# Optimization experiments

Measured on AMD Instinct MI355X. Metric: run time of the kernel, lower is better.

The kernel has to match this reference:

```python
import jax, jax.numpy as jnp
import numpy as np

B, N, IN_F, OUT_F, H = 4, 2048, 256, 256, 8
NH = OUT_F // H  # 32
SLOPE = 0.2
NEG_INF = -9e15


def setup_inputs() -> dict:
    key = jax.random.key(0)
    k1, k2, k3, k4 = jax.random.split(key, 4)
    h = jax.random.normal(k1, (B, N, IN_F), jnp.float32)
    adj = jax.random.randint(k2, (B, N, N), 0, 2).astype(jnp.int32)
    # xavier_uniform with gain 1.414
    gw = 1.414 * np.sqrt(6.0 / (IN_F + H * NH))
    W = jax.random.uniform(k3, (IN_F, H * NH), jnp.float32, -gw, gw)
    ga = 1.414 * np.sqrt(6.0 / (2 * NH + 1))
    a = jax.random.uniform(k4, (2 * NH, 1), jnp.float32, -ga, ga)
    return {"h": h, "adj": adj, "W": W, "a": a}


def reference(h, adj, W, a):
    Wh = h @ W                              # [B, N, H*NH]
    # Faithful to torch .view: raw memory reinterpretation, not a transpose.
    Wh = Wh.reshape(B, H, N, NH)            # [B, H, N, NH]
    Wh1 = Wh @ a[:NH]                       # [B, H, N, 1]
    Wh2 = Wh @ a[NH:]                       # [B, H, N, 1]
    e = Wh1 + jnp.swapaxes(Wh2, 2, 3)       # [B, H, N, N] additive scores
    e = jnp.where(e >= 0, e, SLOPE * e)     # leaky relu
    e = jnp.where(adj[:, None] > 0, e, NEG_INF)
    attn = jax.nn.softmax(e, axis=-1)       # [B, H, N, N]
    h_prime = attn @ Wh                     # [B, H, N, NH]
    h_prime = h_prime.reshape(B, N, OUT_F)  # raw reshape, matches torch .view
    return jax.nn.elu(h_prime)
```

## Files before the change

### kernel.cpp

```cpp
#include <hip/hip_runtime.h>
#include <hip/hip_bf16.h>

#define B_    4
#define N_    2048
#define INF_  256
#define OUTF_ 256
#define H_    8
#define NH_   32
#define BH_   (B_ * H_)
#define ROWS_ (B_ * N_)
#define VSZ_  (N_ * NH_)

typedef float  f32x4 __attribute__((ext_vector_type(4)));
typedef short  s16x8 __attribute__((ext_vector_type(8)));

static __device__ __forceinline__ short f2bf(float x) {
    union { __hip_bfloat16 b; unsigned short u; } cv;
    cv.b = __float2bfloat16(x);
    return (short)cv.u;
}

__global__ __launch_bounds__(256) void hwconv(const float* __restrict__ h,
                                              const float* __restrict__ W,
                                              short* __restrict__ hb,
                                              short* __restrict__ Wf) {
    const int t = blockIdx.x * 256 + threadIdx.x;
    if (blockIdx.x < 1024) {
        const float4* src = (const float4*)(h + (size_t)t * 8);
        float4 v0 = src[0], v1 = src[1];
        float vv[8] = {v0.x, v0.y, v0.z, v0.w, v1.x, v1.y, v1.z, v1.w};
        s16x8 o;
#pragma unroll
        for (int i = 0; i < 8; ++i) o[i] = f2bf(vv[i]);
        *(s16x8*)(hb + (size_t)t * 8) = o;
    } else {
        const int u = t - 1024 * 256;
        const int lane = u & 63, nf = (u >> 6) & 15, kt = u >> 10;
        const float* src = W + (size_t)(kt * 32 + (lane >> 4) * 8) * 256 +
                           nf * 16 + (lane & 15);
        s16x8 o;
#pragma unroll
        for (int i = 0; i < 8; ++i) o[i] = f2bf(src[(size_t)i * 256]);
        *(s16x8*)(Wf + (size_t)u * 8) = o;
    }
}

__global__ __launch_bounds__(256) void gemm_mfma(const short* __restrict__ hb,
                                                 const short* __restrict__ Wf,
                                                 float* __restrict__ Wh) {
    const int bm  = blockIdx.x * 64;
    const int bn4 = blockIdx.y * 4;
    const int tid = threadIdx.x;
    const int wv = tid >> 6, l = tid & 63;
    const int lr = l & 15, lg = l >> 4;
    const int arow = bm + wv * 16 + lr;

    f32x4 acc[4] = {};
    const s16x8* wf = (const s16x8*)Wf;
    const s16x8* ha = (const s16x8*)(hb + (size_t)arow * 256 + lg * 8);

#pragma unroll
    for (int kt = 0; kt < 8; ++kt) {
        s16x8 a = ha[kt * 4];
#pragma unroll
        for (int nf = 0; nf < 4; ++nf) {
            s16x8 b = wf[(size_t)(kt * 16 + bn4 + nf) * 64 + l];
            acc[nf] = __builtin_amdgcn_mfma_f32_16x16x32_bf16(a, b, acc[nf], 0, 0, 0);
        }
    }
#pragma unroll
    for (int nf = 0; nf < 4; ++nf)
#pragma unroll
        for (int r = 0; r < 4; ++r)
            Wh[(size_t)(bm + wv * 16 + 4 * lg + r) * 256 +
               (size_t)(bn4 + nf) * 16 + lr] = acc[nf][r];
}

__global__ __launch_bounds__(256) void st_kernel(const float* __restrict__ Wh,
                                                 const float* __restrict__ a,
                                                 float* __restrict__ s,
                                                 float* __restrict__ t) {
    const int row = blockIdx.x * 256 + threadIdx.x;
    const float* v = Wh + (size_t)row * NH_;
    float s_ = 0.f, t_ = 0.f;
#pragma unroll
    for (int k = 0; k < NH_; k += 4) {
        float4 vv = *(const float4*)(v + k);
        float4 a1 = *(const float4*)(a + k);
        float4 a2 = *(const float4*)(a + NH_ + k);
        s_ += vv.x * a1.x + vv.y * a1.y + vv.z * a1.z + vv.w * a1.w;
        t_ += vv.x * a2.x + vv.y * a2.y + vv.z * a2.z + vv.w * a2.w;
    }
    s[row] = s_;
    t[row] = t_;
}

__global__ __launch_bounds__(256) void vconv(const float* __restrict__ Wh,
                                             short* __restrict__ Vb) {
    const int t = blockIdx.x * 256 + threadIdx.x;
    const int lane = t & 63;
    const int nt   = (t >> 6) & 1;
    const int jt   = (t >> 7) & 63;
    const int bh   = t >> 13;
    const float* src = Wh + (size_t)bh * VSZ_ +
                       (size_t)(jt * 32 + (lane >> 4) * 8) * NH_ +
                       nt * 16 + (lane & 15);
    s16x8 v;
#pragma unroll
    for (int i = 0; i < 8; ++i) v[i] = f2bf(src[(size_t)i * NH_]);
    *(s16x8*)(Vb + (size_t)t * 8) = v;
}

__global__ __launch_bounds__(256) void bitpack(const int* __restrict__ adj,
                                               unsigned int* __restrict__ adjw) {
    const int idx = blockIdx.x * 256 + threadIdx.x;
    const int4* p = (const int4*)(adj + (size_t)idx * 32);
    unsigned int w = 0;
#pragma unroll
    for (int q = 0; q < 8; ++q) {
        int4 v = p[q];
        w |= (v.x != 0 ? 1u : 0u) << (q * 4 + 0);
        w |= (v.y != 0 ? 1u : 0u) << (q * 4 + 1);
        w |= (v.z != 0 ? 1u : 0u) << (q * 4 + 2);
        w |= (v.w != 0 ? 1u : 0u) << (q * 4 + 3);
    }
    adjw[idx] = w;
}

__global__ __launch_bounds__(256) void attn_kernel(const short* __restrict__ Vb,
                                                   const float* __restrict__ s,
                                                   const float* __restrict__ t,
                                                   const unsigned int* __restrict__ adjw,
                                                   float* __restrict__ out) {
    const int bh = blockIdx.y;
    const int b  = bh >> 3;
    const int i0 = blockIdx.x * 64;
    const int tid = threadIdx.x;
    const int wv = tid >> 6;
    const int l  = tid & 63;
    const int lr = l & 15;
    const int lg = l >> 4;

    __shared__ int   adjL[64][68];
    __shared__ float ts[2048];

    {
        const int4* ab = (const int4*)(adjw + (size_t)(b * N_ + i0) * 64);
#pragma unroll
        for (int k = 0; k < 4; ++k) {
            int idx4 = tid + k * 256;
            int4 v = ab[idx4];
            *(int4*)&adjL[idx4 >> 4][(idx4 << 2) & 63] = v;
        }
    }
    {
        const float4* tsrc = (const float4*)(t + (size_t)bh * N_);
        float4 v0 = tsrc[tid];
        float4 v1 = tsrc[tid + 256];
        *(float4*)&ts[tid * 4] = v0;
        *(float4*)&ts[1024 + tid * 4] = v1;
    }
    const float sreg = s[(size_t)bh * N_ + i0 + wv * 16 + lr];
    __syncthreads();

    s16x8 bOnes;
#pragma unroll
    for (int i = 0; i < 8; ++i) bOnes[i] = (lr == 0) ? (short)0x3F80 : (short)0;

    const s16x8* vb = (const s16x8*)(Vb + (size_t)bh * 65536);

    s16x8 nb0 = vb[l];
    s16x8 nb1 = vb[64 + l];
    f32x4 acc0 = {0.f, 0.f, 0.f, 0.f};
    f32x4 acc1 = {0.f, 0.f, 0.f, 0.f};
    f32x4 acc2 = {0.f, 0.f, 0.f, 0.f};

    for (int jt = 0; jt < 64; ++jt) {
        s16x8 b0 = nb0, b1 = nb1;
        if (jt < 63) {
            nb0 = vb[(jt + 1) * 128 + l];
            nb1 = vb[(jt + 1) * 128 + 64 + l];
        }
        const unsigned wsh = ((unsigned)adjL[wv * 16 + lr][jt]) >> (lg * 8);
        float tv[8];
        *(float4*)&tv[0] = *(const float4*)&ts[jt * 32 + lg * 8];
        *(float4*)&tv[4] = *(const float4*)&ts[jt * 32 + lg * 8 + 4];
        s16x8 af;
#pragma unroll
        for (int i = 0; i < 8; ++i) {
            float x = sreg + tv[i];
            x = (wsh & (1u << i)) ? x : -1.0e6f;
            float e = fmaxf(x, 0.2f * x);
            af[i] = f2bf(__expf(e));
        }
        acc0 = __builtin_amdgcn_mfma_f32_16x16x32_bf16(af, b0, acc0, 0, 0, 0);
        acc1 = __builtin_amdgcn_mfma_f32_16x16x32_bf16(af, b1, acc1, 0, 0, 0);
        acc2 = __builtin_amdgcn_mfma_f32_16x16x32_bf16(af, bOnes, acc2, 0, 0, 0);
    }

    float* obase = out + (size_t)bh * VSZ_;
#pragma unroll
    for (int r = 0; r < 4; ++r) {
        const int rloc = 4 * lg + r;
        const float rsum = __shfl(acc2[r], (l & 48));
        const float ir = 1.0f / rsum;
        const int row = i0 + wv * 16 + rloc;
        float v0 = acc0[r] * ir;
        float v1 = acc1[r] * ir;
        v0 = v0 > 0.f ? v0 : expm1f(v0);
        v1 = v1 > 0.f ? v1 : expm1f(v1);
        obase[(size_t)row * NH_ + lr]      = v0;
        obase[(size_t)row * NH_ + 16 + lr] = v1;
    }
}

extern "C" void kernel_launch(void* const* d_in, const int* in_sizes, int n_in,
                              void* d_out, int out_size, void* d_ws, size_t ws_size,
                              hipStream_t stream) {
    const float* h   = (const float*)d_in[0];
    const int*   adj = (const int*)d_in[1];
    const float* W   = (const float*)d_in[2];
    const float* a   = (const float*)d_in[3];
    float* out = (float*)d_out;

    char* ws = (char*)d_ws;
    float* Wh = (float*)ws;
    char*  p1 = ws + (size_t)ROWS_ * OUTF_ * 4;
    float* s  = (float*)p1;
    float* t  = (float*)(p1 + BH_ * N_ * 4);
    unsigned int* adjw = (unsigned int*)(p1 + 2 * BH_ * N_ * 4);
    short* Vb = (short*)(p1 + 2 * BH_ * N_ * 4 + (size_t)B_ * N_ * 64 * 4);
    short* hb = (short*)((char*)Vb + (size_t)BH_ * VSZ_ * 2);
    short* Wf = (short*)((char*)hb + (size_t)ROWS_ * INF_ * 2);

    hwconv<<<1056, 256, 0, stream>>>(h, W, hb, Wf);
    gemm_mfma<<<dim3(ROWS_ / 64, OUTF_ / 64), 256, 0, stream>>>(hb, Wf, Wh);
    st_kernel<<<(BH_ * N_) / 256, 256, 0, stream>>>(Wh, a, s, t);
    vconv<<<(BH_ * N_ * NH_ / 8) / 256, 256, 0, stream>>>(Wh, Vb);
    bitpack<<<(B_ * N_ * (N_ / 32)) / 256, 256, 0, stream>>>(adj, adjw);
    attn_kernel<<<dim3(N_ / 64, BH_), 256, 0, stream>>>(Vb, s, t, adjw, out);
}
```

Before: 166.8 us.

## Factor exp of leaky-relu scores into per-row and per-column products

Precomputes exp(s), exp(0.2s), exp(t) and exp(0.2t) per node, so the attention inner loop evaluates exp(leakyrelu(s+t)) as a max of two products. Because exp is monotonic, this equals the original, and it removes the per-element exponential from the hot loop. It also packs bf16 conversion into v_cvt_pk_bf16_f32 inline asm. The trade-offs are a doubled LDS footprint for the t table and overflow risk, since nothing subtracts a max and large s or t could exceed float range.

```diff
diff --git a/kernel.cpp b/kernel.cpp
--- a/kernel.cpp
+++ b/kernel.cpp
@@ -76,10 +76,10 @@
                (size_t)(bn4 + nf) * 16 + lr] = acc[nf][r];
 }
 
-__global__ __launch_bounds__(256) void st_kernel(const float* __restrict__ Wh,
-                                                 const float* __restrict__ a,
-                                                 float* __restrict__ s,
-                                                 float* __restrict__ t) {
+__global__ __launch_bounds__(256) void st_exp(const float* __restrict__ Wh,
+                                              const float* __restrict__ a,
+                                              float2* __restrict__ sE,
+                                              float2* __restrict__ tE) {
     const int row = blockIdx.x * 256 + threadIdx.x;
     const float* v = Wh + (size_t)row * NH_;
     float s_ = 0.f, t_ = 0.f;
@@ -91,8 +91,8 @@
         s_ += vv.x * a1.x + vv.y * a1.y + vv.z * a1.z + vv.w * a1.w;
         t_ += vv.x * a2.x + vv.y * a2.y + vv.z * a2.z + vv.w * a2.w;
     }
-    s[row] = s_;
-    t[row] = t_;
+    sE[row] = make_float2(__expf(s_), __expf(0.2f * s_));
+    tE[row] = make_float2(__expf(t_), __expf(0.2f * t_));
 }
 
 __global__ __launch_bounds__(256) void vconv(const float* __restrict__ Wh,
@@ -128,8 +128,8 @@
 }
 
 __global__ __launch_bounds__(256) void attn_kernel(const short* __restrict__ Vb,
-                                                   const float* __restrict__ s,
-                                                   const float* __restrict__ t,
+                                                   const float2* __restrict__ sE,
+                                                   const float2* __restrict__ tE,
                                                    const unsigned int* __restrict__ adjw,
                                                    float* __restrict__ out) {
     const int bh = blockIdx.y;
@@ -141,8 +141,8 @@
     const int lr = l & 15;
     const int lg = l >> 4;
 
-    __shared__ int   adjL[64][68];
-    __shared__ float ts[2048];
+    __shared__ int    adjL[64][68];
+    __shared__ float4 ts4[1024];
 
     {
         const int4* ab = (const int4*)(adjw + (size_t)(b * N_ + i0) * 64);
@@ -154,13 +154,11 @@
         }
     }
     {
-        const float4* tsrc = (const float4*)(t + (size_t)bh * N_);
-        float4 v0 = tsrc[tid];
-        float4 v1 = tsrc[tid + 256];
-        *(float4*)&ts[tid * 4] = v0;
-        *(float4*)&ts[1024 + tid * 4] = v1;
-    }
-    const float sreg = s[(size_t)bh * N_ + i0 + wv * 16 + lr];
+        const float4* tsrc = (const float4*)(tE + (size_t)bh * N_);
+#pragma unroll
+        for (int k = 0; k < 4; ++k) ts4[tid + k * 256] = tsrc[tid + k * 256];
+    }
+    const float2 es = sE[(size_t)bh * N_ + i0 + wv * 16 + lr];
     __syncthreads();
 
     s16x8 bOnes;
@@ -182,20 +180,33 @@
             nb1 = vb[(jt + 1) * 128 + 64 + l];
         }
         const unsigned wsh = ((unsigned)adjL[wv * 16 + lr][jt]) >> (lg * 8);
-        float tv[8];
-        *(float4*)&tv[0] = *(const float4*)&ts[jt * 32 + lg * 8];
-        *(float4*)&tv[4] = *(const float4*)&ts[jt * 32 + lg * 8 + 4];
-        s16x8 af;
-#pragma unroll
-        for (int i = 0; i < 8; ++i) {
-            float x = sreg + tv[i];
-            x = (wsh & (1u << i)) ? x : -1.0e6f;
-            float e = fmaxf(x, 0.2f * x);
-            af[i] = f2bf(__expf(e));
-        }
-        acc0 = __builtin_amdgcn_mfma_f32_16x16x32_bf16(af, b0, acc0, 0, 0, 0);
-        acc1 = __builtin_amdgcn_mfma_f32_16x16x32_bf16(af, b1, acc1, 0, 0, 0);
-        acc2 = __builtin_amdgcn_mfma_f32_16x16x32_bf16(af, bOnes, acc2, 0, 0, 0);
+        const int jb = jt * 16 + lg * 4;
+        float4 q0 = ts4[jb + 0];
+        float4 q1 = ts4[jb + 1];
+        float4 q2 = ts4[jb + 2];
+        float4 q3 = ts4[jb + 3];
+        float p[8];
+        p[0] = fmaxf(es.x * q0.x, es.y * q0.y);
+        p[1] = fmaxf(es.x * q0.z, es.y * q0.w);
+        p[2] = fmaxf(es.x * q1.x, es.y * q1.y);
+        p[3] = fmaxf(es.x * q1.z, es.y * q1.w);
+        p[4] = fmaxf(es.x * q2.x, es.y * q2.y);
+        p[5] = fmaxf(es.x * q2.z, es.y * q2.w);
+        p[6] = fmaxf(es.x * q3.x, es.y * q3.y);
+        p[7] = fmaxf(es.x * q3.z, es.y * q3.w);
+#pragma unroll
+        for (int i = 0; i < 8; ++i)
+            if (!((wsh >> i) & 1u)) p[i] = 0.f;
+
+        union { unsigned u[4]; s16x8 v; } af;
+#pragma unroll
+        for (int q = 0; q < 4; ++q)
+            asm("v_cvt_pk_bf16_f32 %0, %1, %2"
+                : "=v"(af.u[q]) : "v"(p[2 * q]), "v"(p[2 * q + 1]));
+
+        acc0 = __builtin_amdgcn_mfma_f32_16x16x32_bf16(af.v, b0, acc0, 0, 0, 0);
+        acc1 = __builtin_amdgcn_mfma_f32_16x16x32_bf16(af.v, b1, acc1, 0, 0, 0);
+        acc2 = __builtin_amdgcn_mfma_f32_16x16x32_bf16(af.v, bOnes, acc2, 0, 0, 0);
     }
 
     float* obase = out + (size_t)bh * VSZ_;
@@ -224,19 +235,19 @@
     float* out = (float*)d_out;
 
     char* ws = (char*)d_ws;
-    float* Wh = (float*)ws;
-    char*  p1 = ws + (size_t)ROWS_ * OUTF_ * 4;
-    float* s  = (float*)p1;
-    float* t  = (float*)(p1 + BH_ * N_ * 4);
-    unsigned int* adjw = (unsigned int*)(p1 + 2 * BH_ * N_ * 4);
-    short* Vb = (short*)(p1 + 2 * BH_ * N_ * 4 + (size_t)B_ * N_ * 64 * 4);
+    float*  Wh = (float*)ws;
+    char*   p1 = ws + (size_t)ROWS_ * OUTF_ * 4;
+    float2* sE = (float2*)p1;
+    float2* tE = (float2*)(p1 + (size_t)BH_ * N_ * 8);
+    unsigned int* adjw = (unsigned int*)(p1 + 2 * (size_t)BH_ * N_ * 8);
+    short* Vb = (short*)(p1 + 2 * (size_t)BH_ * N_ * 8 + (size_t)B_ * N_ * 64 * 4);
     short* hb = (short*)((char*)Vb + (size_t)BH_ * VSZ_ * 2);
     short* Wf = (short*)((char*)hb + (size_t)ROWS_ * INF_ * 2);
 
     hwconv<<<1056, 256, 0, stream>>>(h, W, hb, Wf);
     gemm_mfma<<<dim3(ROWS_ / 64, OUTF_ / 64), 256, 0, stream>>>(hb, Wf, Wh);
-    st_kernel<<<(BH_ * N_) / 256, 256, 0, stream>>>(Wh, a, s, t);
+    st_exp<<<(BH_ * N_) / 256, 256, 0, stream>>>(Wh, a, sE, tE);
     vconv<<<(BH_ * N_ * NH_ / 8) / 256, 256, 0, stream>>>(Wh, Vb);
     bitpack<<<(B_ * N_ * (N_ / 32)) / 256, 256, 0, stream>>>(adj, adjw);
-    attn_kernel<<<dim3(N_ / 64, BH_), 256, 0, stream>>>(Vb, s, t, adjw, out);
-}
+    attn_kernel<<<dim3(N_ / 64, BH_), 256, 0, stream>>>(Vb, sE, tE, adjw, out);
+}
```

Measured after the change: 160.0 us. 4.1% less time.
